# Performance work log

Hardware: AMD Instinct MI355X
Metric: run time of the kernel (lower is better)

Reference implementation:

```python
import jax, jax.numpy as jnp
import numpy as np

N = 30000       # nodes
E = 480000      # edges per graph
NFEAT = 512
NHID = 128
NCLASS = 16
EPS = 0.3       # residual eps from __init__


def _layer(h, d, src, dst, gw, gb):
    """FAGCN-style edge-gated aggregation: a = tanh(W[h_dst;h_src]+b) per edge,
    e = d_dst*d_src*a, z_v = sum_{(u->v)} e * h_u. Dropout is eval-mode (identity)."""
    D = h.shape[1]
    a = jnp.tanh(h[dst] @ gw[:D] + h[src] @ gw[D:] + gb[0])   # [E]
    e = d[dst] * d[src] * a                                    # [E]
    return jax.ops.segment_sum(e[:, None] * h[src], dst, num_segments=h.shape[0])


def setup_inputs():
    key = jax.random.key(0)
    ks = iter(jax.random.split(key, 64))
    def nrm(shape):
        return (jax.random.normal(next(ks), shape) * 0.05).astype(jnp.float32)
    inp = {"x": jax.random.normal(next(ks), (N, NFEAT), dtype=jnp.float32)}
    for i in (1, 2, 3):
        inp[f"src{i}"] = jax.random.randint(next(ks), (E,), 0, N, dtype=jnp.int32)
        inp[f"dst{i}"] = jax.random.randint(next(ks), (E,), 0, N, dtype=jnp.int32)
        inp[f"d{i}"] = jax.random.uniform(next(ks), (N,), minval=0.1, maxval=1.0, dtype=jnp.float32)
    inp["W_t1"] = nrm((NHID, NFEAT)); inp["b_t1"] = jnp.zeros((NHID,), jnp.float32)
    for i in (1, 2, 3):
        inp[f"gW1_{i}"] = nrm((2 * NHID,)); inp[f"gb1_{i}"] = jnp.zeros((1,), jnp.float32)
        inp[f"hw1_{i}"] = nrm((NHID, NHID))
        inp[f"gW2_{i}"] = nrm((6 * NHID,)); inp[f"gb2_{i}"] = jnp.zeros((1,), jnp.float32)
        inp[f"hw2_{i}"] = nrm((3 * NHID, NHID))
    inp["W_t2"] = nrm((NHID, 7 * NHID + NFEAT)); inp["b_t2"] = jnp.zeros((NHID,), jnp.float32)
    inp["W_t3"] = nrm((NCLASS, NHID)); inp["b_t3"] = jnp.zeros((NCLASS,), jnp.float32)
    return inp


def reference(x, src1, dst1, d1, src2, dst2, d2, src3, dst3, d3,
              W_t1, b_t1,
              gW1_1, gb1_1, gW1_2, gb1_2, gW1_3, gb1_3,
              hw1_1, hw1_2, hw1_3,
              gW2_1, gb2_1, gW2_2, gb2_2, gW2_3, gb2_3,
              hw2_1, hw2_2, hw2_3,
              W_t2, b_t2, W_t3, b_t3):
    x = jnp.where(jnp.isnan(x), jnp.zeros_like(x), x)
    raw0 = x
    h = x @ W_t1.T + b_t1                   # t1: nfeat -> nhid
    mid1 = h
    h = jax.nn.relu(h)
    raw1 = h
    h1_1 = jax.nn.relu((EPS * raw1 + _layer(h, d1, src1, dst1, gW1_1, gb1_1)) @ hw1_1)
    h1_2 = jax.nn.relu((EPS * raw1 + _layer(h, d2, src2, dst2, gW1_2, gb1_2)) @ hw1_2)
    h1_3 = jax.nn.relu((EPS * raw1 + _layer(h, d3, src3, dst3, gW1_3, gb1_3)) @ hw1_3)
    h = jnp.concatenate([h1_1, h1_2, h1_3], axis=1)   # [N, 3*nhid]
    raw2 = h
    h2_1 = jax.nn.relu((EPS * raw2 + _layer(h, d1, src1, dst1, gW2_1, gb2_1)) @ hw2_1)
    h2_2 = jax.nn.relu((EPS * raw2 + _layer(h, d2, src2, dst2, gW2_2, gb2_2)) @ hw2_2)
    h2_3 = jax.nn.relu((EPS * raw2 + _layer(h, d3, src3, dst3, gW2_3, gb2_3)) @ hw2_3)
    h = jnp.concatenate([h2_1, h2_2, h2_3, raw1, raw2, raw0], axis=1)  # [N, 7*nhid+nfeat]
    scores = h @ W_t2.T + b_t2
    mid2 = scores
    out = jax.nn.relu(scores) @ W_t3.T + b_t3          # [N, nclass]
    return out, mid1, mid2
```

## Files before the change

### kernel.cpp

```cpp
#include <hip/hip_runtime.h>

#define NN 30000
#define NE 480000
#define EPSV 0.3f

typedef __attribute__((ext_vector_type(4))) float f32x4;
typedef __attribute__((ext_vector_type(8))) short s16x8;
typedef __attribute__((ext_vector_type(4))) short s16x4;

static __device__ __forceinline__ float nclean(float v) { return v != v ? 0.f : v; }
static __device__ __forceinline__ ushort f2bf(float f) {
    uint b = __float_as_uint(f);
    return (ushort)((b + 0x7FFFu + ((b >> 16) & 1u)) >> 16);
}
static __device__ __forceinline__ float bf2f(ushort u) {
    return __uint_as_float(((uint)u) << 16);
}

__global__ __launch_bounds__(256)
void conv_nm(const float* __restrict__ in, ushort* __restrict__ out, int n)
{
    const int i = blockIdx.x * 256 + threadIdx.x;
    if (i < n) out[i] = f2bf(in[i]);
}

__global__ __launch_bounds__(256)
void transpose_w(const float* __restrict__ in, ushort* __restrict__ out, int K)
{
    const int t = blockIdx.x * 256 + threadIdx.x;
    if (t >= K * 128) return;
    const int n = t & 127, k = t >> 7;
    out[(size_t)n * K + k] = f2bf(in[(size_t)k * 128 + n]);
}

__global__ __launch_bounds__(256)
void convert_x(const float* __restrict__ x, ushort* __restrict__ cat)
{
    const int t = blockIdx.x * 256 + threadIdx.x;
    const int v = t >> 7, c4 = (t & 127) * 4;
    const float4 f = *reinterpret_cast<const float4*>(x + (size_t)v * 512 + c4);
    ushort4 o;
    o.x = f2bf(nclean(f.x)); o.y = f2bf(nclean(f.y));
    o.z = f2bf(nclean(f.z)); o.w = f2bf(nclean(f.w));
    *reinterpret_cast<ushort4*>(cat + (size_t)v * 1408 + 896 + c4) = o;
}

static __device__ __forceinline__ s16x8 ldfrag(const ushort* p)
{
    s16x4 lo = *(const s16x4*)p;
    s16x4 hi = *(const s16x4*)(p + 16);
    s16x8 r;
    r[0] = lo[0]; r[1] = lo[1]; r[2] = lo[2]; r[3] = lo[3];
    r[4] = hi[0]; r[5] = hi[1]; r[6] = hi[2]; r[7] = hi[3];
    return r;
}

template<int KTOT, bool BIAS>
__global__ __launch_bounds__(256)
void gemm_mfma(const ushort* __restrict__ A, int lda, int acol,
               const ushort* __restrict__ Bt,
               const float* __restrict__ bias,
               float* __restrict__ outp,
               ushort* __restrict__ outb, int ldb_, int bcol)
{
    __shared__ ushort Asl[32][72];
    __shared__ ushort Bsl[128][72];

    const int tid  = threadIdx.x;
    const int wave = tid >> 6, lane = tid & 63;
    const int l15  = lane & 15, g = lane >> 4;
    const int brow = blockIdx.x * 32;

    f32x4 acc[2][2];
#pragma unroll
    for (int a_ = 0; a_ < 2; a_++)
#pragma unroll
        for (int b_ = 0; b_ < 2; b_++)
#pragma unroll
            for (int i = 0; i < 4; i++) acc[a_][b_][i] = 0.f;

    const int ar = tid >> 3, ac8 = (tid & 7) * 8;
    const int bn = tid >> 1, bc  = (tid & 1) * 32;

    for (int k0 = 0; k0 < KTOT; k0 += 64) {
        s16x8 av = {0, 0, 0, 0, 0, 0, 0, 0};
        if (brow + ar < NN)
            av = *(const s16x8*)(A + (size_t)(brow + ar) * lda + acol + k0 + ac8);
        *(s16x8*)&Asl[ar][ac8] = av;

        const ushort* bsrc = Bt + (size_t)bn * KTOT + k0 + bc;
#pragma unroll
        for (int c = 0; c < 4; c++)
            *(s16x8*)&Bsl[bn][bc + c * 8] = *(const s16x8*)(bsrc + c * 8);
        __syncthreads();

#pragma unroll
        for (int ks = 0; ks < 2; ks++) {
            s16x8 af[2], bfr[2];
#pragma unroll
            for (int rt = 0; rt < 2; rt++)
                af[rt] = ldfrag(&Asl[rt * 16 + l15][ks * 32 + 4 * g]);
#pragma unroll
            for (int ci = 0; ci < 2; ci++)
                bfr[ci] = ldfrag(&Bsl[(2 * wave + ci) * 16 + l15][ks * 32 + 4 * g]);
#pragma unroll
            for (int rt = 0; rt < 2; rt++)
#pragma unroll
                for (int ci = 0; ci < 2; ci++)
                    acc[rt][ci] = __builtin_amdgcn_mfma_f32_16x16x32_bf16(
                        af[rt], bfr[ci], acc[rt][ci], 0, 0, 0);
        }
        __syncthreads();
    }

#pragma unroll
    for (int rt = 0; rt < 2; rt++)
#pragma unroll
        for (int ci = 0; ci < 2; ci++) {
            const int col = (2 * wave + ci) * 16 + l15;
#pragma unroll
            for (int i = 0; i < 4; i++) {
                const int row = brow + rt * 16 + g * 4 + i;
                if (row < NN) {
                    float v = acc[rt][ci][i];
                    if (BIAS) v += bias[col];
                    if (outp) outp[(size_t)row * 128 + col] = v;
                    if (outb) outb[(size_t)row * ldb_ + bcol + col] = f2bf(fmaxf(v, 0.f));
                }
            }
        }
}

template<int D>
__global__ __launch_bounds__(256)
void gate_dots_bf(const ushort* __restrict__ hb, const float* __restrict__ gw,
                  float* __restrict__ hd, float* __restrict__ hs)
{
    const int wv   = (blockIdx.x * 256 + threadIdx.x) >> 6;
    const int lane = threadIdx.x & 63;
    if (wv >= NN) return;
    const uint* row = (const uint*)(hb + (size_t)wv * 1408);
    float sd = 0.f, ss = 0.f;
#pragma unroll
    for (int t = 0; t < D / 128; t++) {
        const int idx = t * 64 + lane;
        const uint u = row[idx];
        const float h0 = bf2f((ushort)(u & 0xffff));
        const float h1 = bf2f((ushort)(u >> 16));
        sd = fmaf(h0, gw[2 * idx], fmaf(h1, gw[2 * idx + 1], sd));
        ss = fmaf(h0, gw[D + 2 * idx], fmaf(h1, gw[D + 2 * idx + 1], ss));
    }
#pragma unroll
    for (int off = 32; off; off >>= 1) {
        sd += __shfl_xor(sd, off);
        ss += __shfl_xor(ss, off);
    }
    if (lane == 0) { hd[wv] = sd; hs[wv] = ss; }
}

__global__ __launch_bounds__(256)
void count_edges(const int* __restrict__ dst, int* __restrict__ cnt)
{
    const int i = blockIdx.x * 256 + threadIdx.x;
    if (i < NE) atomicAdd(&cnt[dst[i]], 1);
}

__global__ __launch_bounds__(1024)
void scan_rowptr(const int* __restrict__ cnt, int* __restrict__ row_ptr,
                 int* __restrict__ cursor)
{
    __shared__ int sdata[1024];
    __shared__ int s_carry;
    const int tid = threadIdx.x;
    if (tid == 0) s_carry = 0;
    __syncthreads();
    for (int base = 0; base < NN; base += 1024) {
        const int i = base + tid;
        const int v = (i < NN) ? cnt[i] : 0;
        sdata[tid] = v;
        __syncthreads();
#pragma unroll
        for (int off = 1; off < 1024; off <<= 1) {
            const int t = (tid >= off) ? sdata[tid - off] : 0;
            __syncthreads();
            sdata[tid] += t;
            __syncthreads();
        }
        const int excl = sdata[tid] - v + s_carry;
        if (i < NN) { row_ptr[i] = excl; cursor[i] = excl; }
        __syncthreads();
        if (tid == 1023) s_carry += sdata[1023];
        __syncthreads();
    }
    if (tid == 0) row_ptr[NN] = s_carry;
}

__global__ __launch_bounds__(256)
void fill_csr(const int* __restrict__ src, const int* __restrict__ dst,
              int* __restrict__ cursor, int* __restrict__ perm_src)
{
    const int i = blockIdx.x * 256 + threadIdx.x;
    if (i < NE) {
        const int pos = atomicAdd(&cursor[dst[i]], 1);
        perm_src[pos] = src[i];
    }
}

__global__ __launch_bounds__(256)
void gather384(const ushort* __restrict__ hb, const float* __restrict__ dv,
               const float* __restrict__ hd, const float* __restrict__ hs,
               const float* __restrict__ gb, const int* __restrict__ rp,
               const int* __restrict__ ps, ushort* __restrict__ zres)
{
    const int lane = threadIdx.x & 63;
    const int v = (blockIdx.x * 256 + threadIdx.x) >> 6;
    const int start = rp[v], end = rp[v + 1];
    const float dvv = dv[v], hdv = hd[v], gb0 = gb[0];
    float4 a0 = {0.f, 0.f, 0.f, 0.f};
    float4 a1 = {0.f, 0.f, 0.f, 0.f};
    for (int chunk = start; chunk < end; chunk += 64) {
        const int nc = min(64, end - chunk);
        float wv_ = 0.f; int sv_ = 0;
        if (lane < nc) {
            const int s = ps[chunk + lane];
            sv_ = s;
            wv_ = dvv * dv[s] * tanhf(hdv + hs[s] + gb0);
        }
        for (int e = 0; e < nc; e++) {
            const float w = __shfl(wv_, e);
            const int   s = __shfl(sv_, e);
            const ushort* hr = hb + (size_t)s * 1408;
            const ushort4 b0 = *(const ushort4*)(hr + 4 * lane);
            a0.x = fmaf(w, bf2f(b0.x), a0.x); a0.y = fmaf(w, bf2f(b0.y), a0.y);
            a0.z = fmaf(w, bf2f(b0.z), a0.z); a0.w = fmaf(w, bf2f(b0.w), a0.w);
            if (lane < 32) {
                const ushort4 b1 = *(const ushort4*)(hr + 256 + 4 * lane);
                a1.x = fmaf(w, bf2f(b1.x), a1.x); a1.y = fmaf(w, bf2f(b1.y), a1.y);
                a1.z = fmaf(w, bf2f(b1.z), a1.z); a1.w = fmaf(w, bf2f(b1.w), a1.w);
            }
        }
    }
    const ushort* hv = hb + (size_t)v * 1408;
    ushort* zr = zres + (size_t)v * 384;
    {
        const ushort4 h0 = *(const ushort4*)(hv + 4 * lane);
        ushort4 o;
        o.x = f2bf(fmaf(EPSV, bf2f(h0.x), a0.x));
        o.y = f2bf(fmaf(EPSV, bf2f(h0.y), a0.y));
        o.z = f2bf(fmaf(EPSV, bf2f(h0.z), a0.z));
        o.w = f2bf(fmaf(EPSV, bf2f(h0.w), a0.w));
        *(ushort4*)(zr + 4 * lane) = o;
    }
    if (lane < 32) {
        const ushort4 h1 = *(const ushort4*)(hv + 256 + 4 * lane);
        ushort4 o;
        o.x = f2bf(fmaf(EPSV, bf2f(h1.x), a1.x));
        o.y = f2bf(fmaf(EPSV, bf2f(h1.y), a1.y));
        o.z = f2bf(fmaf(EPSV, bf2f(h1.z), a1.z));
        o.w = f2bf(fmaf(EPSV, bf2f(h1.w), a1.w));
        *(ushort4*)(zr + 256 + 4 * lane) = o;
    }
}

__global__ __launch_bounds__(256)
void gather128(const ushort* __restrict__ hb, const float* __restrict__ dv,
               const float* __restrict__ hd, const float* __restrict__ hs,
               const float* __restrict__ gb, const int* __restrict__ rp,
               const int* __restrict__ ps, ushort* __restrict__ zres)
{
    const int lane = threadIdx.x & 63;
    const int half = lane >> 5;
    const int c    = lane & 31;
    const int v = (((blockIdx.x * 256 + threadIdx.x) >> 6) << 1) + half;
    const int start = rp[v], end = rp[v + 1];
    const float dvv = dv[v], hdv = hd[v], gb0 = gb[0];
    const int base = half << 5;
    float4 a0 = {0.f, 0.f, 0.f, 0.f};
    for (int chunk = start; chunk < end; chunk += 32) {
        const int nc = min(32, end - chunk);
        float wv_ = 0.f; int sv_ = 0;
        if (c < nc) {
            const int s = ps[chunk + c];
            sv_ = s;
            wv_ = dvv * dv[s] * tanhf(hdv + hs[s] + gb0);
        }
        for (int e = 0; e < nc; e++) {
            const float w = __shfl(wv_, base | e);
            const int   s = __shfl(sv_, base | e);
            const ushort4 b = *(const ushort4*)(hb + (size_t)s * 1408 + 4 * c);
            a0.x = fmaf(w, bf2f(b.x), a0.x); a0.y = fmaf(w, bf2f(b.y), a0.y);
            a0.z = fmaf(w, bf2f(b.z), a0.z); a0.w = fmaf(w, bf2f(b.w), a0.w);
        }
    }
    const ushort4 h0 = *(const ushort4*)(hb + (size_t)v * 1408 + 4 * c);
    ushort4 o;
    o.x = f2bf(fmaf(EPSV, bf2f(h0.x), a0.x));
    o.y = f2bf(fmaf(EPSV, bf2f(h0.y), a0.y));
    o.z = f2bf(fmaf(EPSV, bf2f(h0.z), a0.z));
    o.w = f2bf(fmaf(EPSV, bf2f(h0.w), a0.w));
    *(ushort4*)(zres + (size_t)v * 128 + 4 * c) = o;
}

__global__ __launch_bounds__(256)
void t3_kernel(const float* __restrict__ scores, const float* __restrict__ W3,
               const float* __restrict__ b3, float* __restrict__ out)
{
    const int idx = blockIdx.x * 256 + threadIdx.x;
    const int v = idx >> 4;
    const int c = idx & 15;
    if (v >= NN) return;
    const float4* s4 = reinterpret_cast<const float4*>(scores + (size_t)v * 128);
    const float4* w4 = reinterpret_cast<const float4*>(W3 + (size_t)c * 128);
    float acc = 0.f;
#pragma unroll
    for (int j = 0; j < 32; j++) {
        const float4 s = s4[j];
        const float4 w = w4[j];
        acc = fmaf(fmaxf(s.x, 0.f), w.x, acc);
        acc = fmaf(fmaxf(s.y, 0.f), w.y, acc);
        acc = fmaf(fmaxf(s.z, 0.f), w.z, acc);
        acc = fmaf(fmaxf(s.w, 0.f), w.w, acc);
    }
    out[idx] = acc + b3[c];
}

extern "C" void kernel_launch(void* const* d_in, const int* in_sizes, int n_in,
                              void* d_out, int out_size, void* d_ws, size_t ws_size,
                              hipStream_t stream)
{
    const float* x = (const float*)d_in[0];
    const int*   srcs[3] = {(const int*)d_in[1], (const int*)d_in[4], (const int*)d_in[7]};
    const int*   dsts[3] = {(const int*)d_in[2], (const int*)d_in[5], (const int*)d_in[8]};
    const float* dvs [3] = {(const float*)d_in[3], (const float*)d_in[6], (const float*)d_in[9]};
    const float* W_t1 = (const float*)d_in[10];
    const float* b_t1 = (const float*)d_in[11];
    const float *gW1[3], *gb1[3], *hw1[3], *gW2[3], *gb2[3], *hw2[3];
    for (int j = 0; j < 3; j++) {
        const int b = 12 + j * 6;
        gW1[j] = (const float*)d_in[b + 0];
        gb1[j] = (const float*)d_in[b + 1];
        hw1[j] = (const float*)d_in[b + 2];
        gW2[j] = (const float*)d_in[b + 3];
        gb2[j] = (const float*)d_in[b + 4];
        hw2[j] = (const float*)d_in[b + 5];
    }
    const float* W_t2 = (const float*)d_in[30];
    const float* b_t2 = (const float*)d_in[31];
    const float* W_t3 = (const float*)d_in[32];
    const float* b_t3 = (const float*)d_in[33];

    float* out  = (float*)d_out;
    float* mid1 = out  + (size_t)NN * 16;
    float* mid2 = mid1 + (size_t)NN * 128;

    float*  ws    = (float*)d_ws;
    float*  hd    = ws;
    float*  hs    = hd + NN;
    ushort* zres1 = (ushort*)(hs + NN);
    ushort* zres2 = zres1 + (size_t)NN * 128;
    ushort* cat   = zres2 + (size_t)NN * 384;
    ushort* wt1   = cat + (size_t)NN * 1408;
    ushort* wt2   = wt1 + 128 * 512;
    ushort* hw1t[3], *hw2t[3];
    {
        ushort* p = wt2 + 128 * 1408;
        for (int j = 0; j < 3; j++) { hw1t[j] = p; p += 128 * 128; }
        for (int j = 0; j < 3; j++) { hw2t[j] = p; p += 128 * 384; }
    }
    int* cnt    = (int*)(wt2 + 128 * 1408 + 3 * 128 * 128 + 3 * 128 * 384);
    int* cursor = cnt + NN;
    int* rp[3]; int* psrc[3];
    {
        int* p = cursor + NN;
        for (int j = 0; j < 3; j++) { rp[j] = p; p += NN + 1; }
        for (int j = 0; j < 3; j++) { psrc[j] = p; p += NE; }
    }

    const dim3 blk(256);
    const int GG = (NN + 31) / 32;
    const int WG = (NN * 64 + 255) / 256;
    const int CG = (NE + 255) / 256;

    conv_nm<<<(128 * 512 + 255) / 256, blk, 0, stream>>>(W_t1, wt1, 128 * 512);
    conv_nm<<<(128 * 1408 + 255) / 256, blk, 0, stream>>>(W_t2, wt2, 128 * 1408);
    for (int j = 0; j < 3; j++) {
        transpose_w<<<(128 * 128 + 255) / 256, blk, 0, stream>>>(hw1[j], hw1t[j], 128);
        transpose_w<<<(128 * 384 + 255) / 256, blk, 0, stream>>>(hw2[j], hw2t[j], 384);
    }
    convert_x<<<NN * 128 / 256, blk, 0, stream>>>(x, cat);

    for (int j = 0; j < 3; j++) {
        hipMemsetAsync(cnt, 0, (size_t)NN * sizeof(int), stream);
        count_edges<<<CG, blk, 0, stream>>>(dsts[j], cnt);
        scan_rowptr<<<1, 1024, 0, stream>>>(cnt, rp[j], cursor);
        fill_csr<<<CG, blk, 0, stream>>>(srcs[j], dsts[j], cursor, psrc[j]);
    }

    gemm_mfma<512, true><<<GG, blk, 0, stream>>>(
        cat, 1408, 896, wt1, b_t1, mid1, cat, 1408, 384);

    for (int j = 0; j < 3; j++) {
        gate_dots_bf<128><<<WG, blk, 0, stream>>>(cat + 384, gW1[j], hd, hs);
        gather128<<<NN / 8, blk, 0, stream>>>(cat + 384, dvs[j], hd, hs, gb1[j],
                                              rp[j], psrc[j], zres1);
        gemm_mfma<128, false><<<GG, blk, 0, stream>>>(
            zres1, 128, 0, hw1t[j], nullptr, nullptr, cat, 1408, 512 + j * 128);
    }

    for (int j = 0; j < 3; j++) {
        gate_dots_bf<384><<<WG, blk, 0, stream>>>(cat + 512, gW2[j], hd, hs);
        gather384<<<NN / 4, blk, 0, stream>>>(cat + 512, dvs[j], hd, hs, gb2[j],
                                              rp[j], psrc[j], zres2);
        gemm_mfma<384, false><<<GG, blk, 0, stream>>>(
            zres2, 384, 0, hw2t[j], nullptr, nullptr, cat, 1408, j * 128);
    }

    gemm_mfma<1408, true><<<GG, blk, 0, stream>>>(
        cat, 1408, 0, wt2, b_t2, mid2, nullptr, 0, 0);

    t3_kernel<<<(NN * 16 + 255) / 256, blk, 0, stream>>>(mid2, W_t3, b_t3, out);
}
```

Before: 980.9 us.

## Parallelize CSR row-pointer scan and widen/prefetch gather row loads

Replaces the single-block sequential row-pointer scan with a three-kernel multi-block scan (per-block scan, block-sum scan, fix-up). Rewrites both gather kernels to load 8 bf16 per lane with 16-byte vector loads, using fewer active lanes, and software-prefetches the next neighbor row while accumulating the current one. The aim is to cut the serial scan latency and the memory latency stalls in the edge aggregation, at the cost of extra launches, more registers and idle lanes during loads.

```diff
diff --git a/kernel.cpp b/kernel.cpp
--- a/kernel.cpp
+++ b/kernel.cpp
@@ -3,6 +3,7 @@
 #define NN 30000
 #define NE 480000
 #define EPSV 0.3f
+#define SCAN_B ((NN + 255) / 256)
 
 typedef __attribute__((ext_vector_type(4))) float f32x4;
 typedef __attribute__((ext_vector_type(8))) short s16x8;
@@ -165,34 +166,55 @@
     if (i < NE) atomicAdd(&cnt[dst[i]], 1);
 }
 
-__global__ __launch_bounds__(1024)
-void scan_rowptr(const int* __restrict__ cnt, int* __restrict__ row_ptr,
-                 int* __restrict__ cursor)
-{
-    __shared__ int sdata[1024];
-    __shared__ int s_carry;
-    const int tid = threadIdx.x;
-    if (tid == 0) s_carry = 0;
+__global__ __launch_bounds__(256)
+void scan_part(const int* __restrict__ cnt, int* __restrict__ exc,
+               int* __restrict__ bsum)
+{
+    __shared__ int sd[256];
+    const int t = threadIdx.x;
+    const int i = blockIdx.x * 256 + t;
+    const int val = (i < NN) ? cnt[i] : 0;
+    sd[t] = val;
     __syncthreads();
-    for (int base = 0; base < NN; base += 1024) {
-        const int i = base + tid;
-        const int v = (i < NN) ? cnt[i] : 0;
-        sdata[tid] = v;
-        __syncthreads();
-#pragma unroll
-        for (int off = 1; off < 1024; off <<= 1) {
-            const int t = (tid >= off) ? sdata[tid - off] : 0;
-            __syncthreads();
-            sdata[tid] += t;
-            __syncthreads();
-        }
-        const int excl = sdata[tid] - v + s_carry;
-        if (i < NN) { row_ptr[i] = excl; cursor[i] = excl; }
-        __syncthreads();
-        if (tid == 1023) s_carry += sdata[1023];
-        __syncthreads();
-    }
-    if (tid == 0) row_ptr[NN] = s_carry;
+#pragma unroll
+    for (int off = 1; off < 256; off <<= 1) {
+        const int tmp = (t >= off) ? sd[t - off] : 0;
+        __syncthreads();
+        sd[t] += tmp;
+        __syncthreads();
+    }
+    if (i < NN) exc[i] = sd[t] - val;
+    if (t == 255) bsum[blockIdx.x] = sd[255];
+}
+
+__global__ __launch_bounds__(128)
+void scan_top(int* __restrict__ bsum)
+{
+    __shared__ int sd[128];
+    const int t = threadIdx.x;
+    const int v = (t < SCAN_B) ? bsum[t] : 0;
+    sd[t] = v;
+    __syncthreads();
+#pragma unroll
+    for (int off = 1; off < 128; off <<= 1) {
+        const int tmp = (t >= off) ? sd[t - off] : 0;
+        __syncthreads();
+        sd[t] += tmp;
+        __syncthreads();
+    }
+    if (t < SCAN_B) bsum[t] = sd[t] - v;
+}
+
+__global__ __launch_bounds__(256)
+void scan_fin(const int* __restrict__ exc, const int* __restrict__ bsum,
+              int* __restrict__ rp, int* __restrict__ cursor)
+{
+    const int i = blockIdx.x * 256 + threadIdx.x;
+    if (i < NN) {
+        const int r = exc[i] + bsum[blockIdx.x];
+        rp[i] = r; cursor[i] = r;
+    }
+    if (i == 0) rp[NN] = NE;
 }
 
 __global__ __launch_bounds__(256)
@@ -216,8 +238,9 @@
     const int v = (blockIdx.x * 256 + threadIdx.x) >> 6;
     const int start = rp[v], end = rp[v + 1];
     const float dvv = dv[v], hdv = hd[v], gb0 = gb[0];
-    float4 a0 = {0.f, 0.f, 0.f, 0.f};
-    float4 a1 = {0.f, 0.f, 0.f, 0.f};
+    const bool ld = (lane < 48);
+    float a[8] = {0.f, 0.f, 0.f, 0.f, 0.f, 0.f, 0.f, 0.f};
+
     for (int chunk = start; chunk < end; chunk += 64) {
         const int nc = min(64, end - chunk);
         float wv_ = 0.f; int sv_ = 0;
@@ -226,39 +249,29 @@
             sv_ = s;
             wv_ = dvv * dv[s] * tanhf(hdv + hs[s] + gb0);
         }
+        const int s0 = __shfl(sv_, 0);
+        s16x8 cur = {0, 0, 0, 0, 0, 0, 0, 0};
+        if (ld) cur = *(const s16x8*)(hb + (size_t)s0 * 1408 + 8 * lane);
         for (int e = 0; e < nc; e++) {
             const float w = __shfl(wv_, e);
-            const int   s = __shfl(sv_, e);
-            const ushort* hr = hb + (size_t)s * 1408;
-            const ushort4 b0 = *(const ushort4*)(hr + 4 * lane);
-            a0.x = fmaf(w, bf2f(b0.x), a0.x); a0.y = fmaf(w, bf2f(b0.y), a0.y);
-            a0.z = fmaf(w, bf2f(b0.z), a0.z); a0.w = fmaf(w, bf2f(b0.w), a0.w);
-            if (lane < 32) {
-                const ushort4 b1 = *(const ushort4*)(hr + 256 + 4 * lane);
-                a1.x = fmaf(w, bf2f(b1.x), a1.x); a1.y = fmaf(w, bf2f(b1.y), a1.y);
-                a1.z = fmaf(w, bf2f(b1.z), a1.z); a1.w = fmaf(w, bf2f(b1.w), a1.w);
+            s16x8 nxt = {0, 0, 0, 0, 0, 0, 0, 0};
+            if (e + 1 < nc) {
+                const int s1 = __shfl(sv_, e + 1);
+                if (ld) nxt = *(const s16x8*)(hb + (size_t)s1 * 1408 + 8 * lane);
             }
-        }
-    }
-    const ushort* hv = hb + (size_t)v * 1408;
-    ushort* zr = zres + (size_t)v * 384;
-    {
-        const ushort4 h0 = *(const ushort4*)(hv + 4 * lane);
-        ushort4 o;
-        o.x = f2bf(fmaf(EPSV, bf2f(h0.x), a0.x));
-        o.y = f2bf(fmaf(EPSV, bf2f(h0.y), a0.y));
-        o.z = f2bf(fmaf(EPSV, bf2f(h0.z), a0.z));
-        o.w = f2bf(fmaf(EPSV, bf2f(h0.w), a0.w));
-        *(ushort4*)(zr + 4 * lane) = o;
-    }
-    if (lane < 32) {
-        const ushort4 h1 = *(const ushort4*)(hv + 256 + 4 * lane);
-        ushort4 o;
-        o.x = f2bf(fmaf(EPSV, bf2f(h1.x), a1.x));
-        o.y = f2bf(fmaf(EPSV, bf2f(h1.y), a1.y));
-        o.z = f2bf(fmaf(EPSV, bf2f(h1.z), a1.z));
-        o.w = f2bf(fmaf(EPSV, bf2f(h1.w), a1.w));
-        *(ushort4*)(zr + 256 + 4 * lane) = o;
+#pragma unroll
+            for (int i = 0; i < 8; i++)
+                a[i] = fmaf(w, bf2f((ushort)cur[i]), a[i]);
+            cur = nxt;
+        }
+    }
+    if (ld) {
+        const s16x8 h8 = *(const s16x8*)(hb + (size_t)v * 1408 + 8 * lane);
+        s16x8 o;
+#pragma unroll
+        for (int i = 0; i < 8; i++)
+            o[i] = (short)f2bf(fmaf(EPSV, bf2f((ushort)h8[i]), a[i]));
+        *(s16x8*)(zres + (size_t)v * 384 + 8 * lane) = o;
     }
 }
 
@@ -275,7 +288,9 @@
     const int start = rp[v], end = rp[v + 1];
     const float dvv = dv[v], hdv = hd[v], gb0 = gb[0];
     const int base = half << 5;
-    float4 a0 = {0.f, 0.f, 0.f, 0.f};
+    const bool ld = (c < 16);
+    float a[8] = {0.f, 0.f, 0.f, 0.f, 0.f, 0.f, 0.f, 0.f};
+
     for (int chunk = start; chunk < end; chunk += 32) {
         const int nc = min(32, end - chunk);
         float wv_ = 0.f; int sv_ = 0;
@@ -284,21 +299,30 @@
             sv_ = s;
             wv_ = dvv * dv[s] * tanhf(hdv + hs[s] + gb0);
         }
+        const int s0 = __shfl(sv_, base);
+        s16x8 cur = {0, 0, 0, 0, 0, 0, 0, 0};
+        if (ld) cur = *(const s16x8*)(hb + (size_t)s0 * 1408 + 8 * c);
         for (int e = 0; e < nc; e++) {
             const float w = __shfl(wv_, base | e);
-            const int   s = __shfl(sv_, base | e);
-            const ushort4 b = *(const ushort4*)(hb + (size_t)s * 1408 + 4 * c);
-            a0.x = fmaf(w, bf2f(b.x), a0.x); a0.y = fmaf(w, bf2f(b.y), a0.y);
-            a0.z = fmaf(w, bf2f(b.z), a0.z); a0.w = fmaf(w, bf2f(b.w), a0.w);
-        }
-    }
-    const ushort4 h0 = *(const ushort4*)(hb + (size_t)v * 1408 + 4 * c);
-    ushort4 o;
-    o.x = f2bf(fmaf(EPSV, bf2f(h0.x), a0.x));
-    o.y = f2bf(fmaf(EPSV, bf2f(h0.y), a0.y));
-    o.z = f2bf(fmaf(EPSV, bf2f(h0.z), a0.z));
-    o.w = f2bf(fmaf(EPSV, bf2f(h0.w), a0.w));
-    *(ushort4*)(zres + (size_t)v * 128 + 4 * c) = o;
+            s16x8 nxt = {0, 0, 0, 0, 0, 0, 0, 0};
+            if (e + 1 < nc) {
+                const int s1 = __shfl(sv_, base | (e + 1));
+                if (ld) nxt = *(const s16x8*)(hb + (size_t)s1 * 1408 + 8 * c);
+            }
+#pragma unroll
+            for (int i = 0; i < 8; i++)
+                a[i] = fmaf(w, bf2f((ushort)cur[i]), a[i]);
+            cur = nxt;
+        }
+    }
+    if (ld) {
+        const s16x8 h8 = *(const s16x8*)(hb + (size_t)v * 1408 + 8 * c);
+        s16x8 o;
+#pragma unroll
+        for (int i = 0; i < 8; i++)
+            o[i] = (short)f2bf(fmaf(EPSV, bf2f((ushort)h8[i]), a[i]));
+        *(s16x8*)(zres + (size_t)v * 128 + 8 * c) = o;
+    }
 }
 
 __global__ __launch_bounds__(256)
@@ -370,10 +394,13 @@
     int* cnt    = (int*)(wt2 + 128 * 1408 + 3 * 128 * 128 + 3 * 128 * 384);
     int* cursor = cnt + NN;
     int* rp[3]; int* psrc[3];
+    int* exc; int* bsum;
     {
         int* p = cursor + NN;
         for (int j = 0; j < 3; j++) { rp[j] = p; p += NN + 1; }
         for (int j = 0; j < 3; j++) { psrc[j] = p; p += NE; }
+        exc  = p; p += NN;
+        bsum = p; p += 128;
     }
 
     const dim3 blk(256);
@@ -392,7 +419,9 @@
     for (int j = 0; j < 3; j++) {
         hipMemsetAsync(cnt, 0, (size_t)NN * sizeof(int), stream);
         count_edges<<<CG, blk, 0, stream>>>(dsts[j], cnt);
-        scan_rowptr<<<1, 1024, 0, stream>>>(cnt, rp[j], cursor);
+        scan_part<<<SCAN_B, blk, 0, stream>>>(cnt, exc, bsum);
+        scan_top<<<1, 128, 0, stream>>>(bsum);
+        scan_fin<<<SCAN_B, blk, 0, stream>>>(exc, bsum, rp[j], cursor);
         fill_csr<<<CG, blk, 0, stream>>>(srcs[j], dsts[j], cursor, psrc[j]);
     }
 
```

Result: faster. 828.9 us (-15.5%).
